# Performance work log

Hardware: AMD Instinct MI355X
Metric: run time of the kernel (lower is better)

Reference implementation:

```python
import jax, jax.numpy as jnp
import numpy as np

B, C, H, W = 8, 512, 32, 32
NUM_HEADS = 8
NUM_GROUPS = 32
EPS = 1e-5


def setup_inputs() -> dict:
    key = jax.random.key(0)
    ks = jax.random.split(key, 7)
    x = jax.random.normal(ks[0], (B, C, H, W), dtype=jnp.float32)
    # GroupNorm affine params
    gamma = jnp.ones((C,), dtype=jnp.float32)
    beta = jnp.zeros((C,), dtype=jnp.float32)
    # qkv 1x1 conv1d: weight [3C, C], bias [3C]
    w_qkv = jax.random.normal(ks[1], (3 * C, C), dtype=jnp.float32) * (1.0 / np.sqrt(C))
    b_qkv = jax.random.normal(ks[2], (3 * C,), dtype=jnp.float32) * 0.01
    # proj_out 1x1 conv1d (zero-init in the original; random here so the op is non-trivial)
    w_proj = jax.random.normal(ks[3], (C, C), dtype=jnp.float32) * (1.0 / np.sqrt(C))
    b_proj = jax.random.normal(ks[4], (C,), dtype=jnp.float32) * 0.01
    return {"x": x, "gamma": gamma, "beta": beta, "w_qkv": w_qkv, "b_qkv": b_qkv,
            "w_proj": w_proj, "b_proj": b_proj}


def _group_norm(x, gamma, beta):
    # x: [B, C, L]
    b, c, l = x.shape
    xg = x.reshape(b, NUM_GROUPS, (c // NUM_GROUPS) * l)
    mean = jnp.mean(xg, axis=-1, keepdims=True)
    var = jnp.var(xg, axis=-1, keepdims=True)
    xn = ((xg - mean) * jax.lax.rsqrt(var + EPS)).reshape(b, c, l)
    return xn * gamma[None, :, None] + beta[None, :, None]


def reference(x, gamma, beta, w_qkv, b_qkv, w_proj, b_proj):
    b, c, h, w = x.shape
    L = h * w
    xf = x.reshape(b, c, L)
    xn = _group_norm(xf, gamma, beta)
    # 1x1 conv1d == channel matmul: [B, 3C, L]
    qkv = jnp.einsum('oc,bcl->bol', w_qkv, xn) + b_qkv[None, :, None]
    ch = c // NUM_HEADS  # per-head channels
    q, k, v = jnp.split(qkv, 3, axis=1)
    bh = b * NUM_HEADS
    q = q.reshape(bh, ch, L)
    k = k.reshape(bh, ch, L)
    v = v.reshape(bh, ch, L)
    scale = 1.0 / np.sqrt(np.sqrt(ch))
    weight = jnp.einsum('bct,bcs->bts', q * scale, k * scale)  # [BH, L, L]
    weight = jax.nn.softmax(weight.astype(jnp.float32), axis=-1).astype(q.dtype)
    a = jnp.einsum('bts,bcs->bct', weight, v)  # [BH, ch, L]
    hid = a.reshape(b, c, L)
    hid = jnp.einsum('oc,bcl->bol', w_proj, hid) + b_proj[None, :, None]
    return (xf + hid).reshape(b, c, h, w)
```

## Files before the change

### kernel.cpp

```cpp
#include <hip/hip_runtime.h>

typedef unsigned short u16;
using bf16x8 = __attribute__((ext_vector_type(8))) __bf16;
using f32x4  = __attribute__((ext_vector_type(4))) float;
using f32x16 = __attribute__((ext_vector_type(16))) float;
using u16x8  = __attribute__((ext_vector_type(8))) u16;

constexpr float QSC = 0.180336880111112f;

#define TID ((int)threadIdx.x)

__device__ __forceinline__ float fexp2(float x) { return exp2f(x); }
__device__ __forceinline__ u16 f2bf(float f) {
  __bf16 h = (__bf16)f;
  return __builtin_bit_cast(u16, h);
}
__device__ __forceinline__ unsigned pkbf(float a, float b) {
  return (unsigned)f2bf(a) | ((unsigned)f2bf(b) << 16);
}
__device__ __forceinline__ bf16x8 ldfrag(const u16* p) {
  return __builtin_bit_cast(bf16x8, *(const u16x8*)p);
}
__device__ __forceinline__ int swz(int row, int ch) {
  return ch ^ (row & 7) ^ ((row >> 3) & 7);
}
__device__ __forceinline__ void gload16(const u16* g, u16* l) {
  __builtin_amdgcn_global_load_lds(
      (__attribute__((address_space(1))) void*)g,
      (__attribute__((address_space(3))) void*)l, 16, 0, 0);
}
__device__ __forceinline__ f32x4 mfma16(bf16x8 a, bf16x8 b, f32x4 c) {
  return __builtin_amdgcn_mfma_f32_16x16x32_bf16(a, b, c, 0, 0, 0);
}
__device__ __forceinline__ f32x16 mfma32(bf16x8 a, bf16x8 b, f32x16 c) {
  return __builtin_amdgcn_mfma_f32_32x32x16_bf16(a, b, c, 0, 0, 0);
}

__global__ __launch_bounds__(256) void prep_stats(
    const float* __restrict__ wq, const float* __restrict__ wp,
    u16* __restrict__ wqb, u16* __restrict__ wpb,
    const float* __restrict__ x, float* __restrict__ stats) {
  __shared__ float sm[4], ssm[4];
  int bid = blockIdx.x;
  if (bid < 1024) {
    int i = bid * 256 + TID;
    if (i < 196608) {
      float4 v = ((const float4*)wq)[i];
      u16* o = wqb + i * 4;
      o[0] = f2bf(v.x); o[1] = f2bf(v.y); o[2] = f2bf(v.z); o[3] = f2bf(v.w);
    } else {
      int j = i - 196608;
      float4 v = ((const float4*)wp)[j];
      u16* o = wpb + j * 4;
      o[0] = f2bf(v.x); o[1] = f2bf(v.y); o[2] = f2bf(v.z); o[3] = f2bf(v.w);
    }
    return;
  }
  int blk = bid - 1024;
  size_t base = ((size_t)blk) << 14;
  const float4* xp = (const float4*)(x + base);
  float s = 0.f, ss = 0.f;
#pragma unroll
  for (int i = 0; i < 16; ++i) {
    float4 v = xp[TID + i * 256];
    s += v.x + v.y + v.z + v.w;
    ss += v.x * v.x + v.y * v.y + v.z * v.z + v.w * v.w;
  }
#pragma unroll
  for (int off = 32; off; off >>= 1) {
    s += __shfl_down(s, off);
    ss += __shfl_down(ss, off);
  }
  if ((TID & 63) == 0) { sm[TID >> 6] = s; ssm[TID >> 6] = ss; }
  __syncthreads();
  if (TID == 0) {
    float tot = sm[0] + sm[1] + sm[2] + sm[3];
    float tots = ssm[0] + ssm[1] + ssm[2] + ssm[3];
    float mean = tot * (1.f / 16384.f);
    float var = tots * (1.f / 16384.f) - mean * mean;
    stats[blk * 2] = mean;
    stats[blk * 2 + 1] = rsqrtf(var + 1e-5f);
  }
}

__global__ __launch_bounds__(256) void gn_apply(
    const float* __restrict__ x, const float* __restrict__ gamma,
    const float* __restrict__ beta, const float* __restrict__ stats,
    u16* __restrict__ xnT) {
  __shared__ u16 xt[32 * 520];
  int l0 = blockIdx.x * 32, b = blockIdx.y;
  int li = TID & 31, cb = TID >> 5;
#pragma unroll 4
  for (int it = 0; it < 64; ++it) {
    int c = it * 8 + cb;
    int g = c >> 4;
    float mean = stats[(b * 32 + g) * 2];
    float rstd = stats[(b * 32 + g) * 2 + 1];
    float ga = gamma[c] * rstd;
    float be = beta[c] - mean * ga;
    float v = x[((size_t)b * 512 + c) * 1024 + l0 + li];
    xt[li * 520 + c] = f2bf(v * ga + be);
  }
  __syncthreads();
  int li2 = TID >> 3, u0 = TID & 7;
#pragma unroll
  for (int it = 0; it < 8; ++it) {
    int unit = u0 + it * 8;
    u16x8 v = *(const u16x8*)&xt[li2 * 520 + unit * 8];
    *(u16x8*)&xnT[((size_t)b * 1024 + l0 + li2) * 512 + unit * 8] = v;
  }
}

__global__ __launch_bounds__(256) void qkv_gemm(
    const u16* __restrict__ A, const u16* __restrict__ Bt,
    const float* __restrict__ bias,
    u16* __restrict__ qT, u16* __restrict__ kT, u16* __restrict__ vbuf) {
  __shared__ u16 Al[8192], Bl[8192];
  int lin = blockIdx.x;
  int b = lin & 7;
  int rem = lin >> 3;
  int mi = rem % 12, ni = rem / 12;
  int m0 = mi * 128, n0 = ni * 128;
  int lane = TID & 63, w = TID >> 6;
  int mw = (w >> 1) * 64, nw = (w & 1) * 64;
  const u16* Bb = Bt + (size_t)b * 1024 * 512;
  f32x4 acc[4][4] = {};
  for (int k0 = 0; k0 < 512; k0 += 64) {
#pragma unroll
    for (int u = 0; u < 4; ++u) {
      int unit = u * 256 + TID, row = unit >> 3, ch = unit & 7;
      gload16(&A[(size_t)(m0 + row) * 512 + k0 + swz(row, ch) * 8], &Al[unit * 8]);
      gload16(&Bb[(size_t)(n0 + row) * 512 + k0 + swz(row, ch) * 8], &Bl[unit * 8]);
    }
    __syncthreads();
    bf16x8 xf[4][2];
#pragma unroll
    for (int xi = 0; xi < 4; ++xi)
#pragma unroll
      for (int kf = 0; kf < 2; ++kf) {
        int row = nw + xi * 16 + (lane & 15);
        int lc = kf * 4 + (lane >> 4);
        xf[xi][kf] = ldfrag(&Bl[row * 64 + swz(row, lc) * 8]);
      }
#pragma unroll
    for (int yi = 0; yi < 4; ++yi) {
      int row = mw + yi * 16 + (lane & 15);
      int lc = lane >> 4;
      bf16x8 y0 = ldfrag(&Al[row * 64 + swz(row, lc) * 8]);
      bf16x8 y1 = ldfrag(&Al[row * 64 + swz(row, lc + 4) * 8]);
#pragma unroll
      for (int xi = 0; xi < 4; ++xi) {
        acc[xi][yi] = mfma16(xf[xi][0], y0, acc[xi][yi]);
        acc[xi][yi] = mfma16(xf[xi][1], y1, acc[xi][yi]);
      }
    }
    __syncthreads();
  }
  int sel = m0 >> 9;
  if (sel < 2) {
    u16* dst = sel ? kT : qT;
    int mbase = m0 & 511;
    u16* RP = Al;
    for (int ho = 0; ho < 2; ++ho) {
      if ((w >> 1) == ho) {
#pragma unroll
        for (int xi = 0; xi < 4; ++xi)
#pragma unroll
          for (int yi = 0; yi < 4; ++yi)
#pragma unroll
            for (int r = 0; r < 4; ++r) {
              int lloc = nw + xi * 16 + (lane >> 4) * 4 + r;
              int oc = yi * 16 + (lane & 15);
              float v = acc[xi][yi][r] + bias[m0 + ho * 64 + oc];
              if (sel == 0) v *= QSC;
              RP[lloc * 64 + swz(lloc, oc >> 3) * 8 + (oc & 7)] = f2bf(v);
            }
      }
      __syncthreads();
      int head = (mbase >> 6) + ho;
#pragma unroll
      for (int uu = 0; uu < 4; ++uu) {
        int unit = uu * 256 + TID, row = unit >> 3, ch = unit & 7;
        u16x8 v = *(const u16x8*)&RP[row * 64 + swz(row, ch) * 8];
        *(u16x8*)&dst[((size_t)(b * 8 + head) * 1024 + n0 + row) * 64 + ch * 8] = v;
      }
      __syncthreads();
    }
  } else {
    int mbase = m0 - 1024;
    u16* RP = Al;
    for (int ho = 0; ho < 2; ++ho) {
      if ((w >> 1) == ho) {
#pragma unroll
        for (int xi = 0; xi < 4; ++xi)
#pragma unroll
          for (int yi = 0; yi < 4; ++yi)
#pragma unroll
            for (int r = 0; r < 4; ++r) {
              int lloc = nw + xi * 16 + (lane >> 4) * 4 + r;
              int oc = yi * 16 + (lane & 15);
              float v = acc[xi][yi][r] + bias[m0 + ho * 64 + oc];
              RP[oc * 128 + swz(oc, lloc >> 3) * 8 + (lloc & 7)] = f2bf(v);
            }
      }
      __syncthreads();
      int head = (mbase >> 6) + ho;
#pragma unroll
      for (int uu = 0; uu < 4; ++uu) {
        int unit = uu * 256 + TID, ro = unit >> 4, ch = unit & 15;
        u16x8 v = *(const u16x8*)&RP[ro * 128 + swz(ro, ch) * 8];
        *(u16x8*)&vbuf[((size_t)(b * 8 + head) * 64 + ro) * 1024 + n0 + ch * 8] = v;
      }
      __syncthreads();
    }
  }
}

__global__ __launch_bounds__(256) void attn_mfma(const u16* __restrict__ qT,
                                                 const u16* __restrict__ kT,
                                                 const u16* __restrict__ vb,
                                                 u16* __restrict__ aT) {
  __shared__ u16 smem[16384];
  int lin = blockIdx.x;
  int rem = lin >> 3;
  int bh = (lin & 7) * 8 + (rem >> 3);
  int t0 = (rem & 7) * 128;
  int b = bh >> 3, hd = bh & 7;
  int lane = TID & 63, w = TID >> 6;
  int h = lane >> 5, ln = lane & 31;
  int t = t0 + w * 32 + ln;
  const u16* qp = qT + ((size_t)bh * 1024 + t) * 64;
  const u16* kbase = kT + (size_t)bh * 1024 * 64;
  const u16* vbase = vb + (size_t)bh * 64 * 1024;
  bf16x8 qf[4];
#pragma unroll
  for (int kc = 0; kc < 4; ++kc) qf[kc] = ldfrag(qp + kc * 16 + h * 8);
  float m_r = -1e30f, l_r = 0.f;
  f32x16 oacc[2] = {};

  int u0 = TID, u1 = TID + 256;
  int r0 = u0 >> 3, c0 = u0 & 7;
  int r1 = u1 >> 3, c1 = u1 & 7;
  {
    u16* Ks = smem;
    u16* Vs = smem + 4096;
    gload16(&kbase[(size_t)r0 * 64 + swz(r0, c0) * 8], &Ks[u0 * 8]);
    gload16(&kbase[(size_t)r1 * 64 + swz(r1, c1) * 8], &Ks[u1 * 8]);
    gload16(&vbase[(size_t)r0 * 1024 + swz(r0, c0) * 8], &Vs[u0 * 8]);
    gload16(&vbase[(size_t)r1 * 1024 + swz(r1, c1) * 8], &Vs[u1 * 8]);
  }
  __syncthreads();
  for (int tile = 0; tile < 16; ++tile) {
    const u16* Ks = smem + (tile & 1) * 8192;
    const u16* Vs = Ks + 4096;
    if (tile < 15) {
      int sn = (tile + 1) * 64;
      u16* Kn = smem + ((tile + 1) & 1) * 8192;
      u16* Vn = Kn + 4096;
      gload16(&kbase[(size_t)(sn + r0) * 64 + swz(r0, c0) * 8], &Kn[u0 * 8]);
      gload16(&kbase[(size_t)(sn + r1) * 64 + swz(r1, c1) * 8], &Kn[u1 * 8]);
      gload16(&vbase[(size_t)r0 * 1024 + sn + swz(r0, c0) * 8], &Vn[u0 * 8]);
      gload16(&vbase[(size_t)r1 * 1024 + sn + swz(r1, c1) * 8], &Vn[u1 * 8]);
    }
    f32x16 sacc[2] = {};
    __builtin_amdgcn_s_setprio(1);
#pragma unroll
    for (int sb = 0; sb < 2; ++sb) {
      int srow = sb * 32 + ln;
#pragma unroll
      for (int kc = 0; kc < 4; ++kc) {
        bf16x8 kf = ldfrag(&Ks[srow * 64 + swz(srow, kc * 2 + h) * 8]);
        sacc[sb] = mfma32(kf, qf[kc], sacc[sb]);
      }
    }
    __builtin_amdgcn_s_setprio(0);
    float mp[4];
#pragma unroll
    for (int q = 0; q < 4; ++q) {
      mp[q] = fmaxf(fmaxf(sacc[0][q * 4], sacc[0][q * 4 + 1]),
                    fmaxf(sacc[0][q * 4 + 2], sacc[0][q * 4 + 3]));
      mp[q] = fmaxf(mp[q], fmaxf(fmaxf(sacc[1][q * 4], sacc[1][q * 4 + 1]),
                                 fmaxf(sacc[1][q * 4 + 2], sacc[1][q * 4 + 3])));
    }
    float mx = fmaxf(fmaxf(mp[0], mp[1]), fmaxf(mp[2], mp[3]));
    mx = fmaxf(mx, __shfl_xor(mx, 32));
    bool noresc = (__all(mx <= m_r + 8.f) != 0);
    if (!noresc) {
      float mn = fmaxf(m_r, mx);
      float al = fexp2(m_r - mn);
      m_r = mn;
      l_r *= al;
#pragma unroll
      for (int ca = 0; ca < 2; ++ca)
#pragma unroll
        for (int i = 0; i < 16; ++i) oacc[ca][i] *= al;
    }
    float rp[4] = {0.f, 0.f, 0.f, 0.f};
#pragma unroll
    for (int sb = 0; sb < 2; ++sb)
#pragma unroll
      for (int i = 0; i < 16; ++i) {
        float pv = fexp2(sacc[sb][i] - m_r);
        sacc[sb][i] = pv;
        rp[i & 3] += pv;
      }
    float rs = (rp[0] + rp[1]) + (rp[2] + rp[3]);
    rs += __shfl_xor(rs, 32);
    l_r += rs;
    unsigned W[2][4][2];
#pragma unroll
    for (int sb = 0; sb < 2; ++sb)
#pragma unroll
      for (int p4 = 0; p4 < 4; ++p4)
#pragma unroll
        for (int e = 0; e < 2; ++e)
          W[sb][p4][e] = pkbf(sacc[sb][p4 * 4 + 2 * e], sacc[sb][p4 * 4 + 2 * e + 1]);
#pragma unroll
    for (int m = 0; m < 4; ++m) {
      int sb = m >> 1, q = (m & 1) * 2;
      unsigned a0 = W[sb][q][0], a1 = W[sb][q][1];
      unsigned b0 = W[sb][q + 1][0], b1 = W[sb][q + 1][1];
      unsigned s0w = h ? a0 : b0;
      unsigned s1w = h ? a1 : b1;
      unsigned x0 = (unsigned)__shfl_xor((int)s0w, 32);
      unsigned x1 = (unsigned)__shfl_xor((int)s1w, 32);
      unsigned w0 = h ? x0 : a0;
      unsigned w1 = h ? x1 : a1;
      unsigned w2 = h ? b0 : x0;
      unsigned w3 = h ? b1 : x1;
      uint4 pw = make_uint4(w0, w1, w2, w3);
      bf16x8 pf = __builtin_bit_cast(bf16x8, pw);
      __builtin_amdgcn_s_setprio(1);
#pragma unroll
      for (int ca = 0; ca < 2; ++ca) {
        int crow = ca * 32 + ln;
        bf16x8 vf = ldfrag(&Vs[crow * 64 + swz(crow, m * 2 + h) * 8]);
        oacc[ca] = mfma32(vf, pf, oacc[ca]);
      }
      __builtin_amdgcn_s_setprio(0);
    }
    __syncthreads();
  }
  float rl = 1.f / l_r;
  int tloc = w * 32 + ln;
#pragma unroll
  for (int ca = 0; ca < 2; ++ca)
#pragma unroll
    for (int p4 = 0; p4 < 4; ++p4)
#pragma unroll
      for (int e = 0; e < 2; ++e) {
        int r = p4 * 4 + e * 2;
        int c = ca * 32 + 8 * p4 + 4 * h + 2 * e;
        unsigned pk = pkbf(oacc[ca][r] * rl, oacc[ca][r + 1] * rl);
        *(unsigned*)&smem[tloc * 64 + swz(tloc, c >> 3) * 8 + (c & 7)] = pk;
      }
  __syncthreads();
#pragma unroll
  for (int u = 0; u < 4; ++u) {
    int unit = u * 256 + TID;
    int row = unit >> 3, ch = unit & 7;
    u16x8 v = *(const u16x8*)&smem[row * 64 + swz(row, ch) * 8];
    *(u16x8*)&aT[((size_t)b * 1024 + t0 + row) * 512 + hd * 64 + ch * 8] = v;
  }
}

__global__ __launch_bounds__(256) void proj_gemm(
    const u16* __restrict__ A, const u16* __restrict__ Bt,
    const float* __restrict__ bias, const float* __restrict__ resid,
    float* __restrict__ of) {
  __shared__ u16 Al[8192], Bl[8192];
  int lin = blockIdx.x;
  int b = lin & 7;
  int rem = lin >> 3;
  int mi = rem & 3, ni = rem >> 2;
  int m0 = mi * 128, n0 = ni * 128;
  int lane = TID & 63, w = TID >> 6;
  int mw = (w >> 1) * 64, nw = (w & 1) * 64;
  const u16* Bb = Bt + (size_t)b * 1024 * 512;
  f32x4 acc[4][4] = {};
  for (int k0 = 0; k0 < 512; k0 += 64) {
#pragma unroll
    for (int u = 0; u < 4; ++u) {
      int unit = u * 256 + TID, row = unit >> 3, ch = unit & 7;
      gload16(&A[(size_t)(m0 + row) * 512 + k0 + swz(row, ch) * 8], &Al[unit * 8]);
      gload16(&Bb[(size_t)(n0 + row) * 512 + k0 + swz(row, ch) * 8], &Bl[unit * 8]);
    }
    __syncthreads();
    bf16x8 xf[4][2];
#pragma unroll
    for (int xi = 0; xi < 4; ++xi)
#pragma unroll
      for (int kf = 0; kf < 2; ++kf) {
        int row = mw + xi * 16 + (lane & 15);
        int lc = kf * 4 + (lane >> 4);
        xf[xi][kf] = ldfrag(&Al[row * 64 + swz(row, lc) * 8]);
      }
#pragma unroll
    for (int yi = 0; yi < 4; ++yi) {
      int row = nw + yi * 16 + (lane & 15);
      int lc = lane >> 4;
      bf16x8 y0 = ldfrag(&Bl[row * 64 + swz(row, lc) * 8]);
      bf16x8 y1 = ldfrag(&Bl[row * 64 + swz(row, lc + 4) * 8]);
#pragma unroll
      for (int xi = 0; xi < 4; ++xi) {
        acc[xi][yi] = mfma16(xf[xi][0], y0, acc[xi][yi]);
        acc[xi][yi] = mfma16(xf[xi][1], y1, acc[xi][yi]);
      }
    }
    __syncthreads();
  }
#pragma unroll
  for (int xi = 0; xi < 4; ++xi)
#pragma unroll
    for (int yi = 0; yi < 4; ++yi)
#pragma unroll
      for (int r = 0; r < 4; ++r) {
        int o = m0 + mw + xi * 16 + (lane >> 4) * 4 + r;
        int l = n0 + nw + yi * 16 + (lane & 15);
        size_t idx = ((size_t)b * 512 + o) * 1024 + l;
        of[idx] = acc[xi][yi][r] + bias[o] + resid[idx];
      }
}

extern "C" void kernel_launch(void* const* d_in, const int* in_sizes, int n_in,
                              void* d_out, int out_size, void* d_ws, size_t ws_size,
                              hipStream_t stream) {
  const float* x = (const float*)d_in[0];
  const float* gamma = (const float*)d_in[1];
  const float* beta = (const float*)d_in[2];
  const float* w_qkv = (const float*)d_in[3];
  const float* b_qkv = (const float*)d_in[4];
  const float* w_proj = (const float*)d_in[5];
  const float* b_proj = (const float*)d_in[6];
  float* out = (float*)d_out;

  u16* qT = (u16*)d_ws;
  u16* kT = qT + 4194304;
  u16* vbuf = kT + 4194304;
  u16* aTb = vbuf + 4194304;
  u16* wqb = aTb + 4194304;
  u16* wpb = wqb + 786432;
  float* stats = (float*)(wpb + 262144);
  u16* xnT = (u16*)d_out;

  prep_stats<<<dim3(1280), dim3(256), 0, stream>>>(w_qkv, w_proj, wqb, wpb, x, stats);
  gn_apply<<<dim3(32, 8), dim3(256), 0, stream>>>(x, gamma, beta, stats, xnT);
  qkv_gemm<<<dim3(768), dim3(256), 0, stream>>>(wqb, xnT, b_qkv, qT, kT, vbuf);
  attn_mfma<<<dim3(512), dim3(256), 0, stream>>>(qT, kT, vbuf, aTb);
  proj_gemm<<<dim3(256), dim3(256), 0, stream>>>(wpb, aTb, b_proj, x, out);
}
```

Measured before the change: 100.9 us.

## Use native exp2, packed bf16 convert, permlane swaps, and single-pass QKV epilogue

In the attention kernel, exp2 now uses the hardware builtin, bf16 packing uses v_cvt_pk_bf16_f32 inline asm, and the cross-half max and sum reductions use permlane32_swap instead of shuffles. In the QKV GEMM, both 64-channel halves are staged at once into the two LDS buffers (Al and Bl), which removes the serialized two-pass loop and its extra barriers. The goal is fewer VALU and shuffle instructions in the softmax inner loop and fewer sync points in the epilogue. The raw exp2 builtin skips the denormal and range handling that exp2f performs.

```diff
diff --git a/kernel.cpp b/kernel.cpp
--- a/kernel.cpp
+++ b/kernel.cpp
@@ -5,18 +5,50 @@
 using f32x4  = __attribute__((ext_vector_type(4))) float;
 using f32x16 = __attribute__((ext_vector_type(16))) float;
 using u16x8  = __attribute__((ext_vector_type(8))) u16;
+using u32x2  = __attribute__((ext_vector_type(2))) unsigned;
 
 constexpr float QSC = 0.180336880111112f;
 
 #define TID ((int)threadIdx.x)
 
-__device__ __forceinline__ float fexp2(float x) { return exp2f(x); }
+__device__ __forceinline__ float fexp2(float x) {
+#if __has_builtin(__builtin_amdgcn_exp2f)
+  return __builtin_amdgcn_exp2f(x);
+#else
+  return exp2f(x);
+#endif
+}
 __device__ __forceinline__ u16 f2bf(float f) {
   __bf16 h = (__bf16)f;
   return __builtin_bit_cast(u16, h);
 }
-__device__ __forceinline__ unsigned pkbf(float a, float b) {
-  return (unsigned)f2bf(a) | ((unsigned)f2bf(b) << 16);
+__device__ __forceinline__ unsigned cvtpk(float a, float b) {
+  unsigned r;
+  asm("v_cvt_pk_bf16_f32 %0, %1, %2" : "=v"(r) : "v"(a), "v"(b));
+  return r;
+}
+__device__ __forceinline__ u32x2 plswap(unsigned d, unsigned s) {
+#if __has_builtin(__builtin_amdgcn_permlane32_swap)
+  return __builtin_amdgcn_permlane32_swap(d, s, false, false);
+#else
+  unsigned dx = (unsigned)__shfl_xor((int)d, 32);
+  unsigned sx = (unsigned)__shfl_xor((int)s, 32);
+  int hh = ((int)threadIdx.x >> 5) & 1;
+  u32x2 r;
+  r[0] = hh ? d : sx;
+  r[1] = hh ? dx : s;
+  return r;
+#endif
+}
+__device__ __forceinline__ float xhalf_max(float x) {
+  unsigned u = __builtin_bit_cast(unsigned, x);
+  u32x2 r = plswap(u, u);
+  return fmaxf(__builtin_bit_cast(float, r[0]), __builtin_bit_cast(float, r[1]));
+}
+__device__ __forceinline__ float xhalf_add(float x) {
+  unsigned u = __builtin_bit_cast(unsigned, x);
+  u32x2 r = plswap(u, u);
+  return __builtin_bit_cast(float, r[0]) + __builtin_bit_cast(float, r[1]);
 }
 __device__ __forceinline__ bf16x8 ldfrag(const u16* p) {
   return __builtin_bit_cast(bf16x8, *(const u16x8*)p);
@@ -157,61 +189,53 @@
     __syncthreads();
   }
   int sel = m0 >> 9;
+  int ho = w >> 1;
+  u16* RP = ho ? Bl : Al;
   if (sel < 2) {
+#pragma unroll
+    for (int xi = 0; xi < 4; ++xi)
+#pragma unroll
+      for (int yi = 0; yi < 4; ++yi)
+#pragma unroll
+        for (int r = 0; r < 4; ++r) {
+          int lloc = nw + xi * 16 + (lane >> 4) * 4 + r;
+          int oc = yi * 16 + (lane & 15);
+          float v = acc[xi][yi][r] + bias[m0 + ho * 64 + oc];
+          if (sel == 0) v *= QSC;
+          RP[lloc * 64 + swz(lloc, oc >> 3) * 8 + (oc & 7)] = f2bf(v);
+        }
+    __syncthreads();
     u16* dst = sel ? kT : qT;
-    int mbase = m0 & 511;
-    u16* RP = Al;
-    for (int ho = 0; ho < 2; ++ho) {
-      if ((w >> 1) == ho) {
-#pragma unroll
-        for (int xi = 0; xi < 4; ++xi)
-#pragma unroll
-          for (int yi = 0; yi < 4; ++yi)
-#pragma unroll
-            for (int r = 0; r < 4; ++r) {
-              int lloc = nw + xi * 16 + (lane >> 4) * 4 + r;
-              int oc = yi * 16 + (lane & 15);
-              float v = acc[xi][yi][r] + bias[m0 + ho * 64 + oc];
-              if (sel == 0) v *= QSC;
-              RP[lloc * 64 + swz(lloc, oc >> 3) * 8 + (oc & 7)] = f2bf(v);
-            }
-      }
-      __syncthreads();
-      int head = (mbase >> 6) + ho;
-#pragma unroll
-      for (int uu = 0; uu < 4; ++uu) {
-        int unit = uu * 256 + TID, row = unit >> 3, ch = unit & 7;
-        u16x8 v = *(const u16x8*)&RP[row * 64 + swz(row, ch) * 8];
-        *(u16x8*)&dst[((size_t)(b * 8 + head) * 1024 + n0 + row) * 64 + ch * 8] = v;
-      }
-      __syncthreads();
+    int h0 = (m0 & 511) >> 6;
+#pragma unroll
+    for (int uu = 0; uu < 4; ++uu) {
+      int unit = uu * 256 + TID, row = unit >> 3, ch = unit & 7;
+      u16x8 v0 = *(const u16x8*)&Al[row * 64 + swz(row, ch) * 8];
+      u16x8 v1 = *(const u16x8*)&Bl[row * 64 + swz(row, ch) * 8];
+      *(u16x8*)&dst[((size_t)(b * 8 + h0) * 1024 + n0 + row) * 64 + ch * 8] = v0;
+      *(u16x8*)&dst[((size_t)(b * 8 + h0 + 1) * 1024 + n0 + row) * 64 + ch * 8] = v1;
     }
   } else {
-    int mbase = m0 - 1024;
-    u16* RP = Al;
-    for (int ho = 0; ho < 2; ++ho) {
-      if ((w >> 1) == ho) {
-#pragma unroll
-        for (int xi = 0; xi < 4; ++xi)
-#pragma unroll
-          for (int yi = 0; yi < 4; ++yi)
-#pragma unroll
-            for (int r = 0; r < 4; ++r) {
-              int lloc = nw + xi * 16 + (lane >> 4) * 4 + r;
-              int oc = yi * 16 + (lane & 15);
-              float v = acc[xi][yi][r] + bias[m0 + ho * 64 + oc];
-              RP[oc * 128 + swz(oc, lloc >> 3) * 8 + (lloc & 7)] = f2bf(v);
-            }
-      }
-      __syncthreads();
-      int head = (mbase >> 6) + ho;
-#pragma unroll
-      for (int uu = 0; uu < 4; ++uu) {
-        int unit = uu * 256 + TID, ro = unit >> 4, ch = unit & 15;
-        u16x8 v = *(const u16x8*)&RP[ro * 128 + swz(ro, ch) * 8];
-        *(u16x8*)&vbuf[((size_t)(b * 8 + head) * 64 + ro) * 1024 + n0 + ch * 8] = v;
-      }
-      __syncthreads();
+#pragma unroll
+    for (int xi = 0; xi < 4; ++xi)
+#pragma unroll
+      for (int yi = 0; yi < 4; ++yi)
+#pragma unroll
+        for (int r = 0; r < 4; ++r) {
+          int lloc = nw + xi * 16 + (lane >> 4) * 4 + r;
+          int oc = yi * 16 + (lane & 15);
+          float v = acc[xi][yi][r] + bias[m0 + ho * 64 + oc];
+          RP[oc * 128 + swz(oc, lloc >> 3) * 8 + (lloc & 7)] = f2bf(v);
+        }
+    __syncthreads();
+    int h0 = (m0 - 1024) >> 6;
+#pragma unroll
+    for (int uu = 0; uu < 4; ++uu) {
+      int unit = uu * 256 + TID, ro = unit >> 4, ch = unit & 15;
+      u16x8 v0 = *(const u16x8*)&Al[ro * 128 + swz(ro, ch) * 8];
+      u16x8 v1 = *(const u16x8*)&Bl[ro * 128 + swz(ro, ch) * 8];
+      *(u16x8*)&vbuf[((size_t)(b * 8 + h0) * 64 + ro) * 1024 + n0 + ch * 8] = v0;
+      *(u16x8*)&vbuf[((size_t)(b * 8 + h0 + 1) * 64 + ro) * 1024 + n0 + ch * 8] = v1;
     }
   }
 }
@@ -282,8 +306,7 @@
       mp[q] = fmaxf(mp[q], fmaxf(fmaxf(sacc[1][q * 4], sacc[1][q * 4 + 1]),
                                  fmaxf(sacc[1][q * 4 + 2], sacc[1][q * 4 + 3])));
     }
-    float mx = fmaxf(fmaxf(mp[0], mp[1]), fmaxf(mp[2], mp[3]));
-    mx = fmaxf(mx, __shfl_xor(mx, 32));
+    float mx = xhalf_max(fmaxf(fmaxf(mp[0], mp[1]), fmaxf(mp[2], mp[3])));
     bool noresc = (__all(mx <= m_r + 8.f) != 0);
     if (!noresc) {
       float mn = fmaxf(m_r, mx);
@@ -304,9 +327,7 @@
         sacc[sb][i] = pv;
         rp[i & 3] += pv;
       }
-    float rs = (rp[0] + rp[1]) + (rp[2] + rp[3]);
-    rs += __shfl_xor(rs, 32);
-    l_r += rs;
+    l_r += xhalf_add((rp[0] + rp[1]) + (rp[2] + rp[3]));
     unsigned W[2][4][2];
 #pragma unroll
     for (int sb = 0; sb < 2; ++sb)
@@ -314,7 +335,7 @@
       for (int p4 = 0; p4 < 4; ++p4)
 #pragma unroll
         for (int e = 0; e < 2; ++e)
-          W[sb][p4][e] = pkbf(sacc[sb][p4 * 4 + 2 * e], sacc[sb][p4 * 4 + 2 * e + 1]);
+          W[sb][p4][e] = cvtpk(sacc[sb][p4 * 4 + 2 * e], sacc[sb][p4 * 4 + 2 * e + 1]);
 #pragma unroll
     for (int m = 0; m < 4; ++m) {
       int sb = m >> 1, q = (m & 1) * 2;
@@ -351,7 +372,7 @@
       for (int e = 0; e < 2; ++e) {
         int r = p4 * 4 + e * 2;
         int c = ca * 32 + 8 * p4 + 4 * h + 2 * e;
-        unsigned pk = pkbf(oacc[ca][r] * rl, oacc[ca][r + 1] * rl);
+        unsigned pk = cvtpk(oacc[ca][r] * rl, oacc[ca][r + 1] * rl);
         *(unsigned*)&smem[tloc * 64 + swz(tloc, c >> 3) * 8 + (c & 7)] = pk;
       }
   __syncthreads();
```

New measurement: 87.34 us. -13.4%, faster.
